# Kernel optimization log

Hardware: AMD Instinct MI355X
Metric: run time of the kernel (lower is better)

## Reference

```python
import jax, jax.numpy as jnp
import numpy as np

N_NODES = 50000
N_EDGES = 800000
IN_FEATS = 128
H_FEATS = 256


def setup_inputs() -> dict:
    key = jax.random.key(0)
    ks = jax.random.split(key, 10)
    in_feat = jax.random.normal(ks[0], (N_NODES, IN_FEATS), dtype=jnp.float32)
    src = jax.random.randint(ks[1], (N_EDGES,), 0, N_NODES, dtype=jnp.int32)
    dst = jax.random.randint(ks[2], (N_EDGES,), 0, N_NODES, dtype=jnp.int32)
    s1 = 1.0 / np.sqrt(IN_FEATS)
    s2 = 1.0 / np.sqrt(H_FEATS)
    return {
        "in_feat": in_feat,
        "src": src,
        "dst": dst,
        "W_self1": jax.random.normal(ks[3], (IN_FEATS, H_FEATS), dtype=jnp.float32) * s1,
        "W_neigh1": jax.random.normal(ks[4], (IN_FEATS, H_FEATS), dtype=jnp.float32) * s1,
        "b1": jnp.zeros((H_FEATS,), dtype=jnp.float32),
        "W_self2": jax.random.normal(ks[5], (H_FEATS, H_FEATS), dtype=jnp.float32) * s2,
        "W_neigh2": jax.random.normal(ks[6], (H_FEATS, H_FEATS), dtype=jnp.float32) * s2,
        "b2": jnp.zeros((H_FEATS,), dtype=jnp.float32),
    }


def _sage_conv(h, src, dst, W_self, W_neigh, b, deg_inv):
    # gather neighbor features along edges, mean-reduce into dst nodes
    msg = h[src]                                              # [E, d]
    agg = jax.ops.segment_sum(msg, dst, num_segments=N_NODES)  # [N, d]
    h_neigh = agg * deg_inv                                   # mean aggregation
    return h @ W_self + h_neigh @ W_neigh + b


def reference(in_feat, src, dst, W_self1, W_neigh1, b1, W_self2, W_neigh2, b2):
    # in-degree for mean (zero-degree nodes -> 0 neighbor contribution)
    deg = jax.ops.segment_sum(jnp.ones((N_EDGES,), dtype=jnp.float32), dst,
                              num_segments=N_NODES)
    deg_inv = (1.0 / jnp.maximum(deg, 1.0))[:, None]          # [N, 1]
    h = _sage_conv(in_feat, src, dst, W_self1, W_neigh1, b1, deg_inv)
    h = jax.nn.relu(h)
    h = _sage_conv(h, src, dst, W_self2, W_neigh2, b2, deg_inv)
    return h
```

## Files before the change

### kernel.cpp

```cpp
#include <hip/hip_runtime.h>
#include <hip/hip_bf16.h>
#include <stdint.h>

#define NN 50000
#define NE 800000
#define IN_F 128
#define H_F 256
#define M_PAD 50048

typedef unsigned int uint32;
typedef unsigned short u16;
typedef __attribute__((ext_vector_type(8))) short short8;
typedef __attribute__((ext_vector_type(4))) float floatx4;

__device__ __forceinline__ float bf16_to_f(uint32 bits16) {
    union { uint32 u; float f; } c; c.u = bits16 << 16; return c.f;
}
__device__ __forceinline__ uint32 f_to_bf16(float f) {
    union { float f; uint32 u; } c; c.f = f;
    uint32 u = c.u;
    u += 0x7FFFu + ((u >> 16) & 1u);
    return u >> 16;
}

__device__ __forceinline__ void gload_lds16(const void* g, void* l) {
    __builtin_amdgcn_global_load_lds((__attribute__((address_space(1))) void*)g,
                                     (__attribute__((address_space(3))) void*)l,
                                     16, 0, 0);
}

#define PREP_A (NN * IN_F / 4)
#define PREP_B (256 * 256)
#define PREP_C (256 * 512)
#define PREP_Z (16 + 32)
#define PREP_TOTAL (PREP_A + PREP_B + PREP_C + PREP_Z + NE)

__global__ void prep_kernel(const float* __restrict__ in_feat, u16* __restrict__ inA,
                            const float* __restrict__ Ws1, const float* __restrict__ Wn1,
                            u16* __restrict__ BT1,
                            const float* __restrict__ Ws2, const float* __restrict__ Wn2,
                            u16* __restrict__ BT2,
                            u16* __restrict__ h,
                            const int* __restrict__ dst, int* __restrict__ counts,
                            int* __restrict__ rank) {
    int id = blockIdx.x * 256 + threadIdx.x;
    if (id < PREP_A) {
        float4 v = *((const float4*)in_feat + id);
        ushort4 o;
        o.x = (u16)f_to_bf16(v.x); o.y = (u16)f_to_bf16(v.y);
        o.z = (u16)f_to_bf16(v.z); o.w = (u16)f_to_bf16(v.w);
        *((ushort4*)inA + id) = o;
        return;
    }
    id -= PREP_A;
    if (id < PREP_B) {
        int n = id >> 8, k = id & 255;
        float v = (k < 128) ? Ws1[(size_t)k * H_F + n] : Wn1[(size_t)(k - 128) * H_F + n];
        BT1[(size_t)n * 256 + k] = (u16)f_to_bf16(v);
        return;
    }
    id -= PREP_B;
    if (id < PREP_C) {
        int n = id >> 9, k = id & 511;
        float v = (k < 256) ? Ws2[(size_t)k * H_F + n] : Wn2[(size_t)(k - 256) * H_F + n];
        BT2[(size_t)n * 512 + k] = (u16)f_to_bf16(v);
        return;
    }
    id -= PREP_C;
    if (id < PREP_Z) {
        uint4 z = {0u, 0u, 0u, 0u};
        if (id < 16) *((uint4*)(inA + (size_t)NN * IN_F) + id) = z;
        else         *((uint4*)(h   + (size_t)NN * H_F)  + (id - 16)) = z;
        return;
    }
    id -= PREP_Z;
    if (id < NE) rank[id] = atomicAdd(&counts[dst[id]], 1);
}


__global__ void scan1_kernel(const int* __restrict__ counts, int* __restrict__ row_start,
                             int* __restrict__ partials, int n) {
    __shared__ int s[256];
    int t = threadIdx.x;
    int i = blockIdx.x * 256 + t;
    int x = (i < n) ? counts[i] : 0;
    s[t] = x;
    __syncthreads();
    for (int off = 1; off < 256; off <<= 1) {
        int y = (t >= off) ? s[t - off] : 0;
        __syncthreads();
        s[t] += y;
        __syncthreads();
    }
    if (i < n) row_start[i] = s[t] - x;
    if (t == 255) partials[blockIdx.x] = s[255];
}

__global__ void scan3_kernel(int* __restrict__ row_start, const int* __restrict__ partials,
                             const int* __restrict__ counts,
                             float* __restrict__ deg_inv, int n, int nparts) {
    __shared__ int s[256];
    int t = threadIdx.x;
    int x = (t < nparts) ? partials[t] : 0;
    s[t] = x;
    __syncthreads();
    for (int off = 1; off < 256; off <<= 1) {
        int y = (t >= off) ? s[t - off] : 0;
        __syncthreads();
        s[t] += y;
        __syncthreads();
    }
    int boff = blockIdx.x ? s[blockIdx.x - 1] : 0;
    int i = blockIdx.x * 256 + t;
    if (i >= n) return;
    row_start[i] += boff;
    int c = counts[i];
    deg_inv[i] = 1.0f / (float)(c > 1 ? c : 1);
}

__global__ void scatter_kernel(const int* __restrict__ src, const int* __restrict__ dst,
                               const int* __restrict__ rank, const int* __restrict__ row_start,
                               int* __restrict__ csr_src) {
    int e = blockIdx.x * 256 + threadIdx.x;
    if (e < NE) {
        int d = dst[e];
        csr_src[row_start[d] + rank[e]] = src[e];
    }
}

template<int DW>
__global__ __launch_bounds__(256)
void agg_kernel(const u16* __restrict__ feats, const int* __restrict__ csr_src,
                const int* __restrict__ row_start, const int* __restrict__ counts,
                const float* __restrict__ deg_inv, u16* __restrict__ outp) {
    constexpr int LPR = DW / 4;
    constexpr int EPW = 64 / LPR;
    constexpr int U   = (DW == 64) ? 8 : 16;
    constexpr int EPI = EPW * U;
    const int w = threadIdx.x >> 6, lane = threadIdx.x & 63;
    const int node = blockIdx.x * 4 + w;
    if (node >= NN) return;
    const int start = row_start[node];
    const int cnt   = counts[node];
    const float dinv = deg_inv[node];
    const int g  = lane / LPR;
    const int wo = (lane % LPR) * 4;
    const uint32* ftw = (const uint32*)feats + wo;

    int clampe = cnt > 0 ? cnt - 1 : 0;
    int myidx = csr_src[start + (lane < clampe ? lane : clampe)];
    if (lane >= cnt) myidx = NN;

    float acc[8] = {};
    const int nb = cnt < 64 ? cnt : 64;
    for (int j = 0; j < nb; j += EPI) {
        uint4 x_[U];
#pragma unroll
        for (int u = 0; u < U; ++u) {
            int idx = __shfl(myidx, j + u * EPW + g);
            x_[u] = *(const uint4*)(ftw + (size_t)idx * DW);
        }
#pragma unroll
        for (int u = 0; u < U; ++u) {
            acc[0] += bf16_to_f(x_[u].x & 0xFFFFu); acc[1] += bf16_to_f(x_[u].x >> 16);
            acc[2] += bf16_to_f(x_[u].y & 0xFFFFu); acc[3] += bf16_to_f(x_[u].y >> 16);
            acc[4] += bf16_to_f(x_[u].z & 0xFFFFu); acc[5] += bf16_to_f(x_[u].z >> 16);
            acc[6] += bf16_to_f(x_[u].w & 0xFFFFu); acc[7] += bf16_to_f(x_[u].w >> 16);
        }
    }
    for (int j = 64; j < cnt; j += EPW) {
        int e = j + g;
        int idx = (e < cnt) ? csr_src[start + e] : NN;
        uint4 x = *(const uint4*)(ftw + (size_t)idx * DW);
        acc[0] += bf16_to_f(x.x & 0xFFFFu); acc[1] += bf16_to_f(x.x >> 16);
        acc[2] += bf16_to_f(x.y & 0xFFFFu); acc[3] += bf16_to_f(x.y >> 16);
        acc[4] += bf16_to_f(x.z & 0xFFFFu); acc[5] += bf16_to_f(x.z >> 16);
        acc[6] += bf16_to_f(x.w & 0xFFFFu); acc[7] += bf16_to_f(x.w >> 16);
    }
#pragma unroll
    for (int k = 0; k < 8; ++k) {
        if (LPR <= 16) acc[k] += __shfl_xor(acc[k], 16);
        acc[k] += __shfl_xor(acc[k], 32);
    }
    if (g == 0) {
        uint4 o;
        o.x = f_to_bf16(acc[0] * dinv) | (f_to_bf16(acc[1] * dinv) << 16);
        o.y = f_to_bf16(acc[2] * dinv) | (f_to_bf16(acc[3] * dinv) << 16);
        o.z = f_to_bf16(acc[4] * dinv) | (f_to_bf16(acc[5] * dinv) << 16);
        o.w = f_to_bf16(acc[6] * dinv) | (f_to_bf16(acc[7] * dinv) << 16);
        *(uint4*)((uint32*)outp + (size_t)node * DW + wo) = o;
    }
}

template<int RELU_BF16>
__global__ __launch_bounds__(256)
void gemm_kernel(const u16* __restrict__ A1, const u16* __restrict__ A2, int K1,
                 const u16* __restrict__ BT, const float* __restrict__ bias,
                 void* __restrict__ outp, int M) {
    __shared__ char lds[40960];
    const int tid = threadIdx.x;
    const int w = tid >> 6, lane = tid & 63;
    const int brow = blockIdx.x * 64;
    const int Ktot = 2 * K1;
    const int NT = Ktot >> 6;
    const int T1 = K1 >> 6;
    const int l15 = lane & 15, l7 = lane & 7, kg = lane >> 4;
    const int srow = w * 8 + (lane >> 3);
    const int scb = (lane & 7) * 16;
    const size_t sA = (size_t)K1 * 2;
    const size_t sB = (size_t)Ktot * 2;

    floatx4 acc[4][4] = {};

    for (int kt = 0; kt < NT; ++kt) {
        const char* Ab; int ka;
        if (kt < T1) { Ab = (const char*)A1; ka = kt * 64; }
        else         { Ab = (const char*)A2; ka = (kt - T1) * 64; }
#pragma unroll
        for (int i = 0; i < 2; ++i) {
            int row = i * 32 + srow;
            const char* g = Ab + (size_t)(brow + row) * sA + ka * 2 + (scb ^ ((row & 7) << 4));
            gload_lds16(g, &lds[i * 4096 + w * 1024]);
        }
#pragma unroll
        for (int i = 0; i < 8; ++i) {
            int row = i * 32 + srow;
            const char* g = (const char*)BT + (size_t)row * sB + kt * 128 + (scb ^ ((row & 7) << 4));
            gload_lds16(g, &lds[8192 + i * 4096 + w * 1024]);
        }
        __syncthreads();
#pragma unroll
        for (int kk = 0; kk < 2; ++kk) {
            short8 a[4], b[4];
            const int cbyte = (kk * 64 + kg * 16) ^ (l7 << 4);
#pragma unroll
            for (int m = 0; m < 4; ++m)
                a[m] = *(const short8*)&lds[(m * 16 + l15) * 128 + cbyte];
#pragma unroll
            for (int n = 0; n < 4; ++n)
                b[n] = *(const short8*)&lds[8192 + (w * 64 + n * 16 + l15) * 128 + cbyte];
#pragma unroll
            for (int m = 0; m < 4; ++m)
#pragma unroll
                for (int n = 0; n < 4; ++n)
                    acc[m][n] = __builtin_amdgcn_mfma_f32_16x16x32_bf16(a[m], b[n], acc[m][n], 0, 0, 0);
        }
        __syncthreads();
    }

    const int ocol0 = w * 64;
#pragma unroll
    for (int m = 0; m < 4; ++m) {
#pragma unroll
        for (int j = 0; j < 4; ++j) {
            int row = brow + m * 16 + kg * 4 + j;
            if (row < M) {
#pragma unroll
                for (int n = 0; n < 4; ++n) {
                    int col = ocol0 + n * 16 + l15;
                    float v = acc[m][n][j] + bias[col];
                    if (RELU_BF16) {
                        v = fmaxf(v, 0.0f);
                        ((u16*)outp)[(size_t)row * H_F + col] = (u16)f_to_bf16(v);
                    } else {
                        ((float*)outp)[(size_t)row * H_F + col] = v;
                    }
                }
            }
        }
    }
}


extern "C" void kernel_launch(void* const* d_in, const int* in_sizes, int n_in,
                              void* d_out, int out_size, void* d_ws, size_t ws_size,
                              hipStream_t stream) {
    const float* in_feat  = (const float*)d_in[0];
    const int*   src      = (const int*)d_in[1];
    const int*   dst      = (const int*)d_in[2];
    const float* W_self1  = (const float*)d_in[3];
    const float* W_neigh1 = (const float*)d_in[4];
    const float* b1       = (const float*)d_in[5];
    const float* W_self2  = (const float*)d_in[6];
    const float* W_neigh2 = (const float*)d_in[7];
    const float* b2       = (const float*)d_in[8];
    float* out = (float*)d_out;

    char* p = (char*)d_ws;
    auto alloc = [&](size_t bytes) { char* r = p; p += (bytes + 255) & ~(size_t)255; return r; };
    int*   counts    = (int*)alloc((size_t)NN * 4);
    int*   row_start = (int*)alloc((size_t)NN * 4);
    int*   partials  = (int*)alloc(256 * 4);
    float* deg_inv   = (float*)alloc((size_t)NN * 4);
    int*   rank      = (int*)alloc((size_t)NE * 4);
    int*   csr_src   = (int*)alloc((size_t)NE * 4 + 256);
    u16*   inA       = (u16*)alloc((size_t)M_PAD * IN_F * 2);
    u16*   hn1       = (u16*)alloc((size_t)M_PAD * IN_F * 2);
    u16*   h         = (u16*)alloc((size_t)M_PAD * H_F * 2);
    u16*   hn2       = (u16*)alloc((size_t)M_PAD * H_F * 2);
    u16*   BT1       = (u16*)alloc((size_t)256 * 256 * 2);
    u16*   BT2       = (u16*)alloc((size_t)256 * 512 * 2);

    hipMemsetAsync(counts, 0, (size_t)NN * 4, stream);

    prep_kernel<<<(PREP_TOTAL + 255) / 256, 256, 0, stream>>>(
        in_feat, inA, W_self1, W_neigh1, BT1, W_self2, W_neigh2, BT2, h, dst, counts, rank);

    const int SB = (NN + 255) / 256;
    scan1_kernel<<<SB, 256, 0, stream>>>(counts, row_start, partials, NN);
    scan3_kernel<<<SB, 256, 0, stream>>>(row_start, partials, counts, deg_inv, NN, SB);
    scatter_kernel<<<(NE + 255) / 256, 256, 0, stream>>>(src, dst, rank, row_start, csr_src);

    agg_kernel<IN_F / 2><<<(NN + 3) / 4, 256, 0, stream>>>(inA, csr_src, row_start, counts, deg_inv, hn1);
    gemm_kernel<1><<<M_PAD / 64, 256, 0, stream>>>(inA, hn1, 128, BT1, b1, (void*)h, NN);
    agg_kernel<H_F / 2><<<(NN + 3) / 4, 256, 0, stream>>>(h, csr_src, row_start, counts, deg_inv, hn2);
    gemm_kernel<0><<<M_PAD / 64, 256, 0, stream>>>(h, hn2, 256, BT2, b2, (void*)out, NN);
}
```

Before: 211.9 us.

## Fuse neighbor aggregation into GEMM blocks, keeping aggregated rows in LDS

Merges the per-layer aggregation kernel and the GEMM kernel into one. Each 64-row block first gathers and mean-reduces neighbor features for its own rows into swizzled LDS, then runs the MFMA GEMM, reading the neighbor half of A from LDS instead of from a global hn buffer. This removes the hn1/hn2 writes and reads and two launches. In exchange, each wave handles 16 nodes in sequence, so gather latency is exposed within a block. The GEMM block count is also much smaller than the old aggregation grid, which may reduce parallelism and overlap for the memory-bound gather.

```diff
diff --git a/kernel.cpp b/kernel.cpp
--- a/kernel.cpp
+++ b/kernel.cpp
@@ -128,122 +128,136 @@
     }
 }
 
-template<int DW>
+template<int K1, int RELU_BF16>
 __global__ __launch_bounds__(256)
-void agg_kernel(const u16* __restrict__ feats, const int* __restrict__ csr_src,
-                const int* __restrict__ row_start, const int* __restrict__ counts,
-                const float* __restrict__ deg_inv, u16* __restrict__ outp) {
-    constexpr int LPR = DW / 4;
-    constexpr int EPW = 64 / LPR;
-    constexpr int U   = (DW == 64) ? 8 : 16;
-    constexpr int EPI = EPW * U;
-    const int w = threadIdx.x >> 6, lane = threadIdx.x & 63;
-    const int node = blockIdx.x * 4 + w;
-    if (node >= NN) return;
-    const int start = row_start[node];
-    const int cnt   = counts[node];
-    const float dinv = deg_inv[node];
-    const int g  = lane / LPR;
-    const int wo = (lane % LPR) * 4;
-    const uint32* ftw = (const uint32*)feats + wo;
-
-    int clampe = cnt > 0 ? cnt - 1 : 0;
-    int myidx = csr_src[start + (lane < clampe ? lane : clampe)];
-    if (lane >= cnt) myidx = NN;
-
-    float acc[8] = {};
-    const int nb = cnt < 64 ? cnt : 64;
-    for (int j = 0; j < nb; j += EPI) {
-        uint4 x_[U];
-#pragma unroll
-        for (int u = 0; u < U; ++u) {
-            int idx = __shfl(myidx, j + u * EPW + g);
-            x_[u] = *(const uint4*)(ftw + (size_t)idx * DW);
-        }
-#pragma unroll
-        for (int u = 0; u < U; ++u) {
-            acc[0] += bf16_to_f(x_[u].x & 0xFFFFu); acc[1] += bf16_to_f(x_[u].x >> 16);
-            acc[2] += bf16_to_f(x_[u].y & 0xFFFFu); acc[3] += bf16_to_f(x_[u].y >> 16);
-            acc[4] += bf16_to_f(x_[u].z & 0xFFFFu); acc[5] += bf16_to_f(x_[u].z >> 16);
-            acc[6] += bf16_to_f(x_[u].w & 0xFFFFu); acc[7] += bf16_to_f(x_[u].w >> 16);
-        }
-    }
-    for (int j = 64; j < cnt; j += EPW) {
-        int e = j + g;
-        int idx = (e < cnt) ? csr_src[start + e] : NN;
-        uint4 x = *(const uint4*)(ftw + (size_t)idx * DW);
-        acc[0] += bf16_to_f(x.x & 0xFFFFu); acc[1] += bf16_to_f(x.x >> 16);
-        acc[2] += bf16_to_f(x.y & 0xFFFFu); acc[3] += bf16_to_f(x.y >> 16);
-        acc[4] += bf16_to_f(x.z & 0xFFFFu); acc[5] += bf16_to_f(x.z >> 16);
-        acc[6] += bf16_to_f(x.w & 0xFFFFu); acc[7] += bf16_to_f(x.w >> 16);
-    }
-#pragma unroll
-    for (int k = 0; k < 8; ++k) {
-        if (LPR <= 16) acc[k] += __shfl_xor(acc[k], 16);
-        acc[k] += __shfl_xor(acc[k], 32);
-    }
-    if (g == 0) {
-        uint4 o;
-        o.x = f_to_bf16(acc[0] * dinv) | (f_to_bf16(acc[1] * dinv) << 16);
-        o.y = f_to_bf16(acc[2] * dinv) | (f_to_bf16(acc[3] * dinv) << 16);
-        o.z = f_to_bf16(acc[4] * dinv) | (f_to_bf16(acc[5] * dinv) << 16);
-        o.w = f_to_bf16(acc[6] * dinv) | (f_to_bf16(acc[7] * dinv) << 16);
-        *(uint4*)((uint32*)outp + (size_t)node * DW + wo) = o;
-    }
-}
-
-template<int RELU_BF16>
-__global__ __launch_bounds__(256)
-void gemm_kernel(const u16* __restrict__ A1, const u16* __restrict__ A2, int K1,
-                 const u16* __restrict__ BT, const float* __restrict__ bias,
-                 void* __restrict__ outp, int M) {
-    __shared__ char lds[40960];
+void fused_kernel(const u16* __restrict__ Aft, const int* __restrict__ csr_src,
+                  const int* __restrict__ row_start, const int* __restrict__ counts,
+                  const float* __restrict__ deg_inv,
+                  const u16* __restrict__ BT, const float* __restrict__ bias,
+                  void* __restrict__ outp) {
+    constexpr int ROWB = K1 * 2;
+    constexpr int ANB  = 64 * ROWB;
+    constexpr int DW   = K1 / 2;
+    constexpr int LPR  = DW / 4;
+    constexpr int EPW  = 64 / LPR;
+    constexpr int U    = (K1 == 128) ? 8 : 16;
+    constexpr int EPI  = EPW * U;
+    constexpr int T1   = K1 / 64;
+    constexpr int NT   = 2 * T1;
+
+    __shared__ __attribute__((aligned(16))) char lds[ANB + 8192 + 32768];
+    constexpr int LAS = 0 + ANB;
+    constexpr int LB  = ANB + 8192;
+
     const int tid = threadIdx.x;
     const int w = tid >> 6, lane = tid & 63;
     const int brow = blockIdx.x * 64;
-    const int Ktot = 2 * K1;
-    const int NT = Ktot >> 6;
-    const int T1 = K1 >> 6;
     const int l15 = lane & 15, l7 = lane & 7, kg = lane >> 4;
+    const int g  = lane / LPR;
+    const int wo = (lane % LPR) * 4;
+    const uint32* ftw = (const uint32*)Aft + wo;
+
+    for (int t = 0; t < 16; ++t) {
+        const int r = w * 16 + t;
+        const int node = brow + r;
+        int start = 0, cnt = 0; float dinv = 1.0f;
+        if (node < NN) { start = row_start[node]; cnt = counts[node]; dinv = deg_inv[node]; }
+
+        int clampe = cnt > 0 ? cnt - 1 : 0;
+        int myidx = csr_src[start + (lane < clampe ? lane : clampe)];
+        if (lane >= cnt) myidx = NN;
+
+        float acc[8] = {};
+        const int nb = cnt < 64 ? cnt : 64;
+        for (int j = 0; j < nb; j += EPI) {
+            uint4 x_[U];
+#pragma unroll
+            for (int u = 0; u < U; ++u) {
+                int idx = __shfl(myidx, j + u * EPW + g);
+                x_[u] = *(const uint4*)(ftw + (size_t)idx * DW);
+            }
+#pragma unroll
+            for (int u = 0; u < U; ++u) {
+                acc[0] += bf16_to_f(x_[u].x & 0xFFFFu); acc[1] += bf16_to_f(x_[u].x >> 16);
+                acc[2] += bf16_to_f(x_[u].y & 0xFFFFu); acc[3] += bf16_to_f(x_[u].y >> 16);
+                acc[4] += bf16_to_f(x_[u].z & 0xFFFFu); acc[5] += bf16_to_f(x_[u].z >> 16);
+                acc[6] += bf16_to_f(x_[u].w & 0xFFFFu); acc[7] += bf16_to_f(x_[u].w >> 16);
+            }
+        }
+        for (int j = 64; j < cnt; j += EPW) {
+            int e = j + g;
+            int idx = (e < cnt) ? csr_src[start + e] : NN;
+            uint4 x = *(const uint4*)(ftw + (size_t)idx * DW);
+            acc[0] += bf16_to_f(x.x & 0xFFFFu); acc[1] += bf16_to_f(x.x >> 16);
+            acc[2] += bf16_to_f(x.y & 0xFFFFu); acc[3] += bf16_to_f(x.y >> 16);
+            acc[4] += bf16_to_f(x.z & 0xFFFFu); acc[5] += bf16_to_f(x.z >> 16);
+            acc[6] += bf16_to_f(x.w & 0xFFFFu); acc[7] += bf16_to_f(x.w >> 16);
+        }
+#pragma unroll
+        for (int k = 0; k < 8; ++k) {
+            if (LPR <= 16) acc[k] += __shfl_xor(acc[k], 16);
+            acc[k] += __shfl_xor(acc[k], 32);
+        }
+        if (g == 0) {
+            uint4 o;
+            o.x = f_to_bf16(acc[0] * dinv) | (f_to_bf16(acc[1] * dinv) << 16);
+            o.y = f_to_bf16(acc[2] * dinv) | (f_to_bf16(acc[3] * dinv) << 16);
+            o.z = f_to_bf16(acc[4] * dinv) | (f_to_bf16(acc[5] * dinv) << 16);
+            o.w = f_to_bf16(acc[6] * dinv) | (f_to_bf16(acc[7] * dinv) << 16);
+            int cb = wo * 4;
+            *(uint4*)&lds[r * ROWB + (cb ^ ((r & 7) << 4))] = o;
+        }
+    }
+    __syncthreads();
+
     const int srow = w * 8 + (lane >> 3);
     const int scb = (lane & 7) * 16;
-    const size_t sA = (size_t)K1 * 2;
-    const size_t sB = (size_t)Ktot * 2;
-
-    floatx4 acc[4][4] = {};
+    const size_t sB = (size_t)(2 * K1) * 2;
+
+    floatx4 acc2[4][4] = {};
+    const char* Ab = (const char*)Aft + (size_t)brow * ROWB;
 
     for (int kt = 0; kt < NT; ++kt) {
-        const char* Ab; int ka;
-        if (kt < T1) { Ab = (const char*)A1; ka = kt * 64; }
-        else         { Ab = (const char*)A2; ka = (kt - T1) * 64; }
-#pragma unroll
-        for (int i = 0; i < 2; ++i) {
-            int row = i * 32 + srow;
-            const char* g = Ab + (size_t)(brow + row) * sA + ka * 2 + (scb ^ ((row & 7) << 4));
-            gload_lds16(g, &lds[i * 4096 + w * 1024]);
+        if (kt < T1) {
+#pragma unroll
+            for (int i = 0; i < 2; ++i) {
+                int row = i * 32 + srow;
+                const char* gp = Ab + (size_t)row * ROWB + kt * 128 + (scb ^ ((row & 7) << 4));
+                gload_lds16(gp, &lds[LAS + i * 4096 + w * 1024]);
+            }
         }
 #pragma unroll
         for (int i = 0; i < 8; ++i) {
             int row = i * 32 + srow;
-            const char* g = (const char*)BT + (size_t)row * sB + kt * 128 + (scb ^ ((row & 7) << 4));
-            gload_lds16(g, &lds[8192 + i * 4096 + w * 1024]);
+            const char* gp = (const char*)BT + (size_t)row * sB + kt * 128 + (scb ^ ((row & 7) << 4));
+            gload_lds16(gp, &lds[LB + i * 4096 + w * 1024]);
         }
         __syncthreads();
 #pragma unroll
         for (int kk = 0; kk < 2; ++kk) {
+            const int cbyte = kk * 64 + kg * 16;
             short8 a[4], b[4];
-            const int cbyte = (kk * 64 + kg * 16) ^ (l7 << 4);
+            if (kt < T1) {
+#pragma unroll
+                for (int m = 0; m < 4; ++m)
+                    a[m] = *(const short8*)&lds[LAS + (m * 16 + l15) * 128 + (cbyte ^ (l7 << 4))];
+            } else {
+#pragma unroll
+                for (int m = 0; m < 4; ++m) {
+                    int r = m * 16 + l15;
+                    a[m] = *(const short8*)&lds[r * ROWB + (((kt - T1) * 128 + cbyte) ^ (l7 << 4))];
+                }
+            }
+#pragma unroll
+            for (int n = 0; n < 4; ++n) {
+                int rb = w * 64 + n * 16 + l15;
+                b[n] = *(const short8*)&lds[LB + rb * 128 + (cbyte ^ (l7 << 4))];
+            }
 #pragma unroll
             for (int m = 0; m < 4; ++m)
-                a[m] = *(const short8*)&lds[(m * 16 + l15) * 128 + cbyte];
-#pragma unroll
-            for (int n = 0; n < 4; ++n)
-                b[n] = *(const short8*)&lds[8192 + (w * 64 + n * 16 + l15) * 128 + cbyte];
-#pragma unroll
-            for (int m = 0; m < 4; ++m)
 #pragma unroll
                 for (int n = 0; n < 4; ++n)
-                    acc[m][n] = __builtin_amdgcn_mfma_f32_16x16x32_bf16(a[m], b[n], acc[m][n], 0, 0, 0);
+                    acc2[m][n] = __builtin_amdgcn_mfma_f32_16x16x32_bf16(a[m], b[n], acc2[m][n], 0, 0, 0);
         }
         __syncthreads();
     }
@@ -254,11 +268,11 @@
 #pragma unroll
         for (int j = 0; j < 4; ++j) {
             int row = brow + m * 16 + kg * 4 + j;
-            if (row < M) {
+            if (row < NN) {
 #pragma unroll
                 for (int n = 0; n < 4; ++n) {
                     int col = ocol0 + n * 16 + l15;
-                    float v = acc[m][n][j] + bias[col];
+                    float v = acc2[m][n][j] + bias[col];
                     if (RELU_BF16) {
                         v = fmaxf(v, 0.0f);
                         ((u16*)outp)[(size_t)row * H_F + col] = (u16)f_to_bf16(v);
@@ -295,9 +309,7 @@
     int*   rank      = (int*)alloc((size_t)NE * 4);
     int*   csr_src   = (int*)alloc((size_t)NE * 4 + 256);
     u16*   inA       = (u16*)alloc((size_t)M_PAD * IN_F * 2);
-    u16*   hn1       = (u16*)alloc((size_t)M_PAD * IN_F * 2);
     u16*   h         = (u16*)alloc((size_t)M_PAD * H_F * 2);
-    u16*   hn2       = (u16*)alloc((size_t)M_PAD * H_F * 2);
     u16*   BT1       = (u16*)alloc((size_t)256 * 256 * 2);
     u16*   BT2       = (u16*)alloc((size_t)256 * 512 * 2);
 
@@ -311,8 +323,8 @@
     scan3_kernel<<<SB, 256, 0, stream>>>(row_start, partials, counts, deg_inv, NN, SB);
     scatter_kernel<<<(NE + 255) / 256, 256, 0, stream>>>(src, dst, rank, row_start, csr_src);
 
-    agg_kernel<IN_F / 2><<<(NN + 3) / 4, 256, 0, stream>>>(inA, csr_src, row_start, counts, deg_inv, hn1);
-    gemm_kernel<1><<<M_PAD / 64, 256, 0, stream>>>(inA, hn1, 128, BT1, b1, (void*)h, NN);
-    agg_kernel<H_F / 2><<<(NN + 3) / 4, 256, 0, stream>>>(h, csr_src, row_start, counts, deg_inv, hn2);
-    gemm_kernel<0><<<M_PAD / 64, 256, 0, stream>>>(h, hn2, 256, BT2, b2, (void*)out, NN);
-}
+    fused_kernel<IN_F, 1><<<M_PAD / 64, 256, 0, stream>>>(
+        inA, csr_src, row_start, counts, deg_inv, BT1, b1, (void*)h);
+    fused_kernel<H_F, 0><<<M_PAD / 64, 256, 0, stream>>>(
+        h, csr_src, row_start, counts, deg_inv, BT2, b2, (void*)out);
+}
```

Measured after the change: 242.7 us. 14.6% more time.

## Quantize node features to int8 with per-row scales before neighbor aggregation

Applied to the files above, without the earlier changes.

Adds a per-row int8 quantization pass (absmax scale, offset-128 encoding) over the bf16 feature tables, and rewrites the aggregation kernel to gather the int8 rows and dequantize on the fly. The offset is removed at the end using the summed scales. This halves the bytes fetched per gathered neighbor row in the memory-bound gather, at the cost of two extra quantization kernels and reduced numerical precision in the aggregated features. The unrolled first-block loop now assumes a single pass of up to 64 edges, so its trip count depends on the lane-per-row count.

```diff
diff --git a/kernel.cpp b/kernel.cpp
--- a/kernel.cpp
+++ b/kernel.cpp
@@ -128,15 +128,51 @@
     }
 }
 
-template<int DW>
+template<int F>
 __global__ __launch_bounds__(256)
-void agg_kernel(const u16* __restrict__ feats, const int* __restrict__ csr_src,
-                const int* __restrict__ row_start, const int* __restrict__ counts,
-                const float* __restrict__ deg_inv, u16* __restrict__ outp) {
-    constexpr int LPR = DW / 4;
+void quant_kernel(const u16* __restrict__ in, uint32* __restrict__ q8,
+                  float* __restrict__ qs, int nrows) {
+    constexpr int VPL = F / 64;
+    const int w = threadIdx.x >> 6, lane = threadIdx.x & 63;
+    const int row = blockIdx.x * 4 + w;
+    if (row >= nrows) return;
+    float v[VPL];
+    if (VPL == 2) {
+        uint32 x = *(const uint32*)(in + (size_t)row * F + lane * 2);
+        v[0] = bf16_to_f(x & 0xFFFFu); v[1] = bf16_to_f(x >> 16);
+    } else {
+        uint2 x = *(const uint2*)(in + (size_t)row * F + lane * 4);
+        v[0] = bf16_to_f(x.x & 0xFFFFu); v[1] = bf16_to_f(x.x >> 16);
+        v[2] = bf16_to_f(x.y & 0xFFFFu); v[3] = bf16_to_f(x.y >> 16);
+    }
+    float m = 0.0f;
+#pragma unroll
+    for (int k = 0; k < VPL; ++k) m = fmaxf(m, fabsf(v[k]));
+#pragma unroll
+    for (int d = 1; d < 64; d <<= 1) m = fmaxf(m, __shfl_xor(m, d));
+    float s  = m * (1.0f / 127.0f);
+    float rs = (m > 0.0f) ? 127.0f / m : 0.0f;
+    if (lane == 0) qs[row] = s;
+    uint32 o = 0;
+#pragma unroll
+    for (int k = 0; k < VPL; ++k) {
+        int q = (int)rintf(v[k] * rs) + 128;
+        o |= ((uint32)(q & 0xFF)) << (8 * k);
+    }
+    if (VPL == 4) q8[(size_t)row * (F / 4) + lane] = o;
+    else *(u16*)((char*)q8 + (size_t)row * F + lane * 2) = (u16)(o & 0xFFFFu);
+}
+
+template<int F>
+__global__ __launch_bounds__(256)
+void agg8_kernel(const uint32* __restrict__ q8, const float* __restrict__ qs,
+                 const int* __restrict__ csr_src, const int* __restrict__ row_start,
+                 const int* __restrict__ counts, const float* __restrict__ deg_inv,
+                 u16* __restrict__ outp) {
+    constexpr int WPR = F / 4;
+    constexpr int LPR = F / 16;
     constexpr int EPW = 64 / LPR;
-    constexpr int U   = (DW == 64) ? 8 : 16;
-    constexpr int EPI = EPW * U;
+    constexpr int U   = (F == 128) ? 8 : 16;
     const int w = threadIdx.x >> 6, lane = threadIdx.x & 63;
     const int node = blockIdx.x * 4 + w;
     if (node >= NN) return;
@@ -145,50 +181,67 @@
     const float dinv = deg_inv[node];
     const int g  = lane / LPR;
     const int wo = (lane % LPR) * 4;
-    const uint32* ftw = (const uint32*)feats + wo;
+    const uint32* ftw = q8 + wo;
 
     int clampe = cnt > 0 ? cnt - 1 : 0;
     int myidx = csr_src[start + (lane < clampe ? lane : clampe)];
     if (lane >= cnt) myidx = NN;
-
-    float acc[8] = {};
-    const int nb = cnt < 64 ? cnt : 64;
-    for (int j = 0; j < nb; j += EPI) {
-        uint4 x_[U];
+    float s_all = qs[myidx];
+
+    float acc[16] = {};
+    float ssum = 0.0f;
+    {
+        uint4 x_[U]; float s_[U];
 #pragma unroll
         for (int u = 0; u < U; ++u) {
-            int idx = __shfl(myidx, j + u * EPW + g);
-            x_[u] = *(const uint4*)(ftw + (size_t)idx * DW);
+            int idx = __shfl(myidx, u * EPW + g);
+            s_[u] = __shfl(s_all, u * EPW + g);
+            x_[u] = *(const uint4*)(ftw + (size_t)idx * WPR);
         }
 #pragma unroll
         for (int u = 0; u < U; ++u) {
-            acc[0] += bf16_to_f(x_[u].x & 0xFFFFu); acc[1] += bf16_to_f(x_[u].x >> 16);
-            acc[2] += bf16_to_f(x_[u].y & 0xFFFFu); acc[3] += bf16_to_f(x_[u].y >> 16);
-            acc[4] += bf16_to_f(x_[u].z & 0xFFFFu); acc[5] += bf16_to_f(x_[u].z >> 16);
-            acc[6] += bf16_to_f(x_[u].w & 0xFFFFu); acc[7] += bf16_to_f(x_[u].w >> 16);
+            ssum += s_[u];
+            const uint32 ww[4] = {x_[u].x, x_[u].y, x_[u].z, x_[u].w};
+#pragma unroll
+            for (int t = 0; t < 4; ++t)
+#pragma unroll
+                for (int b = 0; b < 4; ++b)
+                    acc[t * 4 + b] += s_[u] * (float)((ww[t] >> (8 * b)) & 0xFFu);
         }
     }
     for (int j = 64; j < cnt; j += EPW) {
         int e = j + g;
         int idx = (e < cnt) ? csr_src[start + e] : NN;
-        uint4 x = *(const uint4*)(ftw + (size_t)idx * DW);
-        acc[0] += bf16_to_f(x.x & 0xFFFFu); acc[1] += bf16_to_f(x.x >> 16);
-        acc[2] += bf16_to_f(x.y & 0xFFFFu); acc[3] += bf16_to_f(x.y >> 16);
-        acc[4] += bf16_to_f(x.z & 0xFFFFu); acc[5] += bf16_to_f(x.z >> 16);
-        acc[6] += bf16_to_f(x.w & 0xFFFFu); acc[7] += bf16_to_f(x.w >> 16);
-    }
-#pragma unroll
-    for (int k = 0; k < 8; ++k) {
-        if (LPR <= 16) acc[k] += __shfl_xor(acc[k], 16);
-        acc[k] += __shfl_xor(acc[k], 32);
+        uint4 x = *(const uint4*)(ftw + (size_t)idx * WPR);
+        float s = qs[idx];
+        ssum += s;
+        const uint32 ww[4] = {x.x, x.y, x.z, x.w};
+#pragma unroll
+        for (int t = 0; t < 4; ++t)
+#pragma unroll
+            for (int b = 0; b < 4; ++b)
+                acc[t * 4 + b] += s * (float)((ww[t] >> (8 * b)) & 0xFFu);
+    }
+#pragma unroll
+    for (int d = LPR; d < 64; d <<= 1) {
+#pragma unroll
+        for (int k = 0; k < 16; ++k) acc[k] += __shfl_xor(acc[k], d);
+        ssum += __shfl_xor(ssum, d);
     }
     if (g == 0) {
-        uint4 o;
-        o.x = f_to_bf16(acc[0] * dinv) | (f_to_bf16(acc[1] * dinv) << 16);
-        o.y = f_to_bf16(acc[2] * dinv) | (f_to_bf16(acc[3] * dinv) << 16);
-        o.z = f_to_bf16(acc[4] * dinv) | (f_to_bf16(acc[5] * dinv) << 16);
-        o.w = f_to_bf16(acc[6] * dinv) | (f_to_bf16(acc[7] * dinv) << 16);
-        *(uint4*)((uint32*)outp + (size_t)node * DW + wo) = o;
+        const float bias = 128.0f * ssum;
+        uint4 o0, o1;
+        o0.x = f_to_bf16((acc[0]  - bias) * dinv) | (f_to_bf16((acc[1]  - bias) * dinv) << 16);
+        o0.y = f_to_bf16((acc[2]  - bias) * dinv) | (f_to_bf16((acc[3]  - bias) * dinv) << 16);
+        o0.z = f_to_bf16((acc[4]  - bias) * dinv) | (f_to_bf16((acc[5]  - bias) * dinv) << 16);
+        o0.w = f_to_bf16((acc[6]  - bias) * dinv) | (f_to_bf16((acc[7]  - bias) * dinv) << 16);
+        o1.x = f_to_bf16((acc[8]  - bias) * dinv) | (f_to_bf16((acc[9]  - bias) * dinv) << 16);
+        o1.y = f_to_bf16((acc[10] - bias) * dinv) | (f_to_bf16((acc[11] - bias) * dinv) << 16);
+        o1.z = f_to_bf16((acc[12] - bias) * dinv) | (f_to_bf16((acc[13] - bias) * dinv) << 16);
+        o1.w = f_to_bf16((acc[14] - bias) * dinv) | (f_to_bf16((acc[15] - bias) * dinv) << 16);
+        uint32* op = (uint32*)outp + (size_t)node * (F / 2) + wo * 2;
+        *(uint4*)op = o0;
+        *(uint4*)(op + 4) = o1;
     }
 }
 
@@ -288,18 +341,22 @@
 
     char* p = (char*)d_ws;
     auto alloc = [&](size_t bytes) { char* r = p; p += (bytes + 255) & ~(size_t)255; return r; };
-    int*   counts    = (int*)alloc((size_t)NN * 4);
-    int*   row_start = (int*)alloc((size_t)NN * 4);
-    int*   partials  = (int*)alloc(256 * 4);
-    float* deg_inv   = (float*)alloc((size_t)NN * 4);
-    int*   rank      = (int*)alloc((size_t)NE * 4);
-    int*   csr_src   = (int*)alloc((size_t)NE * 4 + 256);
-    u16*   inA       = (u16*)alloc((size_t)M_PAD * IN_F * 2);
-    u16*   hn1       = (u16*)alloc((size_t)M_PAD * IN_F * 2);
-    u16*   h         = (u16*)alloc((size_t)M_PAD * H_F * 2);
-    u16*   hn2       = (u16*)alloc((size_t)M_PAD * H_F * 2);
-    u16*   BT1       = (u16*)alloc((size_t)256 * 256 * 2);
-    u16*   BT2       = (u16*)alloc((size_t)256 * 512 * 2);
+    int*    counts    = (int*)alloc((size_t)NN * 4);
+    int*    row_start = (int*)alloc((size_t)NN * 4);
+    int*    partials  = (int*)alloc(256 * 4);
+    float*  deg_inv   = (float*)alloc((size_t)NN * 4);
+    int*    rank      = (int*)alloc((size_t)NE * 4);
+    int*    csr_src   = (int*)alloc((size_t)NE * 4 + 256);
+    u16*    inA       = (u16*)alloc((size_t)M_PAD * IN_F * 2);
+    u16*    hn1       = (u16*)alloc((size_t)M_PAD * IN_F * 2);
+    u16*    h         = (u16*)alloc((size_t)M_PAD * H_F * 2);
+    u16*    hn2       = (u16*)alloc((size_t)M_PAD * H_F * 2);
+    u16*    BT1       = (u16*)alloc((size_t)256 * 256 * 2);
+    u16*    BT2       = (u16*)alloc((size_t)256 * 512 * 2);
+    uint32* inA8      = (uint32*)alloc((size_t)(NN + 1) * IN_F);
+    float*  sIn       = (float*)alloc((size_t)(NN + 1) * 4);
+    uint32* h8        = (uint32*)alloc((size_t)(NN + 1) * H_F);
+    float*  sH        = (float*)alloc((size_t)(NN + 1) * 4);
 
     hipMemsetAsync(counts, 0, (size_t)NN * 4, stream);
 
@@ -311,8 +368,11 @@
     scan3_kernel<<<SB, 256, 0, stream>>>(row_start, partials, counts, deg_inv, NN, SB);
     scatter_kernel<<<(NE + 255) / 256, 256, 0, stream>>>(src, dst, rank, row_start, csr_src);
 
-    agg_kernel<IN_F / 2><<<(NN + 3) / 4, 256, 0, stream>>>(inA, csr_src, row_start, counts, deg_inv, hn1);
+    const int QB = (NN + 1 + 3) / 4;
+    quant_kernel<IN_F><<<QB, 256, 0, stream>>>(inA, inA8, sIn, NN + 1);
+    agg8_kernel<IN_F><<<(NN + 3) / 4, 256, 0, stream>>>(inA8, sIn, csr_src, row_start, counts, deg_inv, hn1);
     gemm_kernel<1><<<M_PAD / 64, 256, 0, stream>>>(inA, hn1, 128, BT1, b1, (void*)h, NN);
-    agg_kernel<H_F / 2><<<(NN + 3) / 4, 256, 0, stream>>>(h, csr_src, row_start, counts, deg_inv, hn2);
+    quant_kernel<H_F><<<QB, 256, 0, stream>>>(h, h8, sH, NN + 1);
+    agg8_kernel<H_F><<<(NN + 3) / 4, 256, 0, stream>>>(h8, sH, csr_src, row_start, counts, deg_inv, hn2);
     gemm_kernel<0><<<M_PAD / 64, 256, 0, stream>>>(h, hn2, 256, BT2, b2, (void*)out, NN);
 }
```

New measurement: 268.8 us. 26.9% more time.
